# Performance work log

Hardware: AMD Instinct MI355X
Metric: run time of the kernel (lower is better)

The kernel has to match this reference:

```python
import jax, jax.numpy as jnp
import numpy as np

N_NODES = 50000
N_EDGES = 800000
IN_SIZE = 128
HID = 128
OUT_SIZE = 64
N_LAYERS = 2
MAXK = 32


def setup_inputs() -> dict:
    key = jax.random.key(0)
    ks = jax.random.split(key, 8)
    s = 0.05  # small init scale, xavier-like
    return {
        "x": jax.random.normal(ks[0], (N_NODES, IN_SIZE), dtype=jnp.float32),
        "W_in": jax.random.normal(ks[1], (IN_SIZE, HID), dtype=jnp.float32) * s,
        "b_in": jnp.zeros((HID,), dtype=jnp.float32),
        "W_self": jax.random.normal(ks[2], (N_LAYERS, HID, HID), dtype=jnp.float32) * s,
        "W_neigh": jax.random.normal(ks[3], (N_LAYERS, HID, HID), dtype=jnp.float32) * s,
        "W_out": jax.random.normal(ks[4], (HID, OUT_SIZE), dtype=jnp.float32) * s,
        "b_out": jnp.zeros((OUT_SIZE,), dtype=jnp.float32),
        "edge_index": jax.random.randint(ks[5], (2, N_EDGES), 0, N_NODES, dtype=jnp.int32),
        "k": MAXK,
    }


def _maxk(x, k):
    # Keep top-k values per row, zero out the rest (MaxK nonlinearity).
    vals, idx = jax.lax.top_k(x, k)                     # [N, k]
    rows = jnp.arange(x.shape[0])[:, None]
    return jnp.zeros_like(x).at[rows, idx].set(vals)


def reference(x, W_in, b_in, W_self, W_neigh, W_out, b_out, edge_index, k):
    N = x.shape[0]
    src, dst = edge_index[0], edge_index[1]
    # Row sums of the (src->dst) adjacency = out-degree of src, per original code.
    deg = jax.ops.segment_sum(jnp.ones((src.shape[0],), dtype=x.dtype), src,
                              num_segments=N)[:, None]  # [N, 1]
    h = x @ W_in + b_in                                  # lin_in
    for i in range(W_self.shape[0]):
        hs = _maxk(h, k)                                 # MaxK sparsify [N, H]
        # adj @ hs : out[i] = sum over edges (i -> j) of hs[j]; then mean-normalize
        agg = jax.ops.segment_sum(hs[dst], src, num_segments=N) / (deg + 1e-6)
        h = hs @ W_self[i] + agg @ W_neigh[i]            # h_self + h_neigh
        # dropout (eval) and Identity norm are no-ops
    return h @ W_out + b_out                             # lin_out
```

## Files before the change

kernel.cpp:

```cpp
#include <hip/hip_runtime.h>

#define KDIM 128
#define NNODE 50000
#define CHSTRIDE 800000

typedef _Float16 f16x8 __attribute__((ext_vector_type(8)));
typedef _Float16 f16x4 __attribute__((ext_vector_type(4)));
typedef float f32x16 __attribute__((ext_vector_type(16)));

#define NRANGE 6250
#define ECHUNK 3200

__global__ void hist_kernel(const int* __restrict__ src, int* __restrict__ cnt, int E) {
    const int r = blockIdx.x & 7;
    const int chunk = blockIdx.x >> 3;
    const int lo = r * NRANGE, hi = lo + NRANGE;
    const int base = chunk * ECHUNK;
    const int end = min(base + ECHUNK, E);
    for (int i = base + threadIdx.x; i < end; i += 256) {
        int s = src[i];
        if (s >= lo && s < hi) atomicAdd(&cnt[s], 1);
    }
}

__global__ void scatter_kernel(const int* __restrict__ src, const int* __restrict__ dst,
                               int* cursor, int* __restrict__ col, int E) {
    const int r = blockIdx.x & 7;
    const int chunk = blockIdx.x >> 3;
    const int lo = r * NRANGE, hi = lo + NRANGE;
    const int base = chunk * ECHUNK;
    const int end = min(base + ECHUNK, E);
    for (int i = base + threadIdx.x; i < end; i += 256) {
        int s = src[i];
        if (s >= lo && s < hi) {
            int p = atomicAdd(&cursor[s], 1);
            col[p] = dst[i];
        }
    }
}

__global__ void scan1_kernel(const int* __restrict__ cnt, int* __restrict__ row_ptr,
                             int* __restrict__ bsum, int N) {
    __shared__ int ws[4];
    const int t = threadIdx.x;
    const int lane = t & 63, w = t >> 6;
    const int i = blockIdx.x * 256 + t;
    int v = (i < N) ? cnt[i] : 0;
    int x = v;
    #pragma unroll
    for (int off = 1; off < 64; off <<= 1) {
        int u = __shfl_up(x, off);
        if (lane >= off) x += u;
    }
    if (lane == 63) ws[w] = x;
    __syncthreads();
    int wexcl = 0;
    #pragma unroll
    for (int k = 0; k < 4; k++) wexcl += (k < w) ? ws[k] : 0;
    if (i < N) row_ptr[i] = wexcl + x - v;
    if (t == 255) bsum[blockIdx.x] = wexcl + x;
}

__global__ void scan2_kernel(int* __restrict__ bsum, int NB) {
    __shared__ int ws[4];
    const int t = threadIdx.x;
    const int lane = t & 63, w = t >> 6;
    int v = (t < NB) ? bsum[t] : 0;
    int x = v;
    #pragma unroll
    for (int off = 1; off < 64; off <<= 1) {
        int u = __shfl_up(x, off);
        if (lane >= off) x += u;
    }
    if (lane == 63) ws[w] = x;
    __syncthreads();
    int wexcl = 0;
    #pragma unroll
    for (int k = 0; k < 4; k++) wexcl += (k < w) ? ws[k] : 0;
    if (t < NB) bsum[t] = wexcl + x - v;
}

__global__ void scan3_kernel(const int* __restrict__ bsum, int* __restrict__ row_ptr,
                             int* __restrict__ cursor, int N, int E) {
    const int i = blockIdx.x * 256 + threadIdx.x;
    if (i < N) {
        int v = row_ptr[i] + bsum[blockIdx.x];
        row_ptr[i] = v;
        cursor[i] = v;
    }
    if (i == 0) row_ptr[N] = E;
}

__global__ void sortrows_kernel(const int* __restrict__ row_ptr, int* __restrict__ col, int M) {
    int wid = (blockIdx.x * blockDim.x + threadIdx.x) >> 6;
    int lane = threadIdx.x & 63;
    if (wid >= M) return;
    int s = row_ptr[wid], e = row_ptr[wid + 1], len = e - s;
    if (len <= 1) return;
    if (len <= 64) {
        int v = (lane < len) ? col[s + lane] : 0x7fffffff;
        #pragma unroll
        for (int k = 2; k <= 64; k <<= 1) {
            #pragma unroll
            for (int j = k >> 1; j > 0; j >>= 1) {
                int o = __shfl_xor(v, j);
                bool dir = ((lane & k) == 0);
                bool smaller = ((lane & j) == 0);
                int mn = min(v, o), mx = max(v, o);
                v = (dir == smaller) ? mn : mx;
            }
        }
        if (lane < len) col[s + lane] = v;
    } else if (lane == 0) {
        for (int a = s + 1; a < e; a++) {
            int key = col[a];
            int b = a - 1;
            while (b >= s && col[b] > key) { col[b + 1] = col[b]; b--; }
            col[b + 1] = key;
        }
    }
}

__device__ __forceinline__ float2 maxk_row(float2 v, int lane) {
    unsigned int u0 = __float_as_uint(v.x);
    u0 = (u0 & 0x80000000u) ? ~u0 : (u0 | 0x80000000u);
    unsigned int u1 = __float_as_uint(v.y);
    u1 = (u1 & 0x80000000u) ? ~u1 : (u1 | 0x80000000u);

    unsigned int prefix = 0;
    int remaining = 32;
    #pragma unroll
    for (int b = 31; b >= 0; --b) {
        unsigned int candHi = (prefix >> b) | 1u;
        unsigned long long m0 = __ballot((u0 >> b) == candHi);
        unsigned long long m1 = __ballot((u1 >> b) == candHi);
        int cnt = __popcll(m0) + __popcll(m1);
        if (cnt >= remaining) prefix |= (1u << b);
        else remaining -= cnt;
    }

    unsigned long long e0 = __ballot(u0 == prefix);
    unsigned long long e1 = __ballot(u1 == prefix);
    unsigned long long g0 = __ballot(u0 > prefix);
    unsigned long long g1 = __ballot(u1 > prefix);
    int quota = 32 - (__popcll(g0) + __popcll(g1));
    unsigned long long below = (1ULL << lane) - 1ULL;
    int rank0 = __popcll(e0 & below) + __popcll(e1 & below);
    int rank1 = rank0 + (int)((e0 >> lane) & 1ULL);
    bool k0 = (u0 > prefix) || (((e0 >> lane) & 1ULL) && rank0 < quota);
    bool k1 = (u1 > prefix) || (((e1 >> lane) & 1ULL) && rank1 < quota);

    float2 o;
    o.x = k0 ? v.x : 0.0f;
    o.y = k1 ? v.y : 0.0f;
    return o;
}

#define ANPB 16
#define AECAP 1024

__global__ __launch_bounds__(256)
void aggregate_kernel(const float* __restrict__ hsc, const int* __restrict__ row_ptr,
                      const int* __restrict__ col, float* __restrict__ agg, int M) {
    __shared__ int cols[AECAP];
    const int c = blockIdx.x & 7;
    const int g = blockIdx.x >> 3;
    const int n0 = g * ANPB;
    const int tid = threadIdx.x;
    const int w = tid >> 6;
    const int lane = tid & 63;
    const int ng = lane >> 4;
    const int e2 = (lane >> 3) & 1;
    const int f2 = lane & 7;

    const int nend = min(n0 + ANPB, M);
    const int base0 = row_ptr[n0];
    const int ecount = row_ptr[nend] - base0;
    const bool fits = (ecount <= AECAP);
    if (fits) {
        for (int i = tid; i < ecount; i += 256) cols[i] = col[base0 + i];
    }
    __syncthreads();

    const int n = n0 + w * 4 + ng;
    const bool valid = (n < M);
    const int s = valid ? (row_ptr[n] - base0) : 0;
    const int e = valid ? (row_ptr[n + 1] - base0) : 0;
    const char* bp = (const char*)(hsc + (size_t)c * CHSTRIDE) + f2 * 8;

    float ax = 0.f, ay = 0.f, bx = 0.f, by = 0.f;
    int j = s + e2;
    if (fits) {
        for (; j + 2 < e; j += 4) {
            unsigned o0 = (unsigned)cols[j] << 6;
            unsigned o1 = (unsigned)cols[j + 2] << 6;
            float2 v0 = *(const float2*)(bp + o0);
            float2 v1 = *(const float2*)(bp + o1);
            ax += v0.x; ay += v0.y;
            bx += v1.x; by += v1.y;
        }
        if (j < e) {
            float2 v = *(const float2*)(bp + ((unsigned)cols[j] << 6));
            ax += v.x; ay += v.y;
        }
    } else {
        const int* cg = col + base0;
        for (; j + 2 < e; j += 4) {
            unsigned o0 = (unsigned)cg[j] << 6;
            unsigned o1 = (unsigned)cg[j + 2] << 6;
            float2 v0 = *(const float2*)(bp + o0);
            float2 v1 = *(const float2*)(bp + o1);
            ax += v0.x; ay += v0.y;
            bx += v1.x; by += v1.y;
        }
        if (j < e) {
            float2 v = *(const float2*)(bp + ((unsigned)cg[j] << 6));
            ax += v.x; ay += v.y;
        }
    }

    float tx = ax + bx, ty = ay + by;
    tx += __shfl_xor(tx, 8);
    ty += __shfl_xor(ty, 8);
    if (valid && e2 == 0) {
        float inv = 1.0f / ((float)(e - s) + 1e-6f);
        float2 o;
        o.x = tx * inv;
        o.y = ty * inv;
        ((float2*)(agg + (size_t)n * KDIM + c * 16))[f2] = o;
    }
}

__global__ void conv_wt_kernel(const float* __restrict__ W_in,
                               const float* __restrict__ W_self,
                               const float* __restrict__ W_neigh,
                               const float* __restrict__ W_out,
                               _Float16* __restrict__ wb) {
    int t = blockIdx.x * blockDim.x + threadIdx.x;
    if (t < 81920) {
        int m = t >> 14;
        int e = t & 16383;
        int n = e >> 7, k = e & 127;
        const float* S = (m == 0) ? W_in
                       : (m <= 2) ? (W_self + (size_t)(m - 1) * 16384)
                                  : (W_neigh + (size_t)(m - 3) * 16384);
        float v = S[k * 128 + n];
        _Float16 hi = (_Float16)v;
        _Float16 lo = (_Float16)(v - (float)hi);
        int pair = m * 2;
        wb[(size_t)pair * 16384 + n * 128 + k] = hi;
        wb[(size_t)(pair + 1) * 16384 + n * 128 + k] = lo;
    } else if (t < 90112) {
        int e = t - 81920;
        int n = e >> 7, k = e & 127;
        float v = W_out[k * 64 + n];
        _Float16 hi = (_Float16)v;
        _Float16 lo = (_Float16)(v - (float)hi);
        wb[(size_t)10 * 16384 + e] = hi;
        wb[(size_t)11 * 16384 + e] = lo;
    }
}

template <int BN, bool DUAL, bool BIAS, bool A1CHUNK, bool FUSE_MAXK, bool FUSE_OUT>
__global__ __launch_bounds__(256)
void gemm_mfma(const float* __restrict__ A1, const float* __restrict__ A2,
               const _Float16* __restrict__ B1h, const _Float16* __restrict__ B1l,
               const _Float16* __restrict__ B2h, const _Float16* __restrict__ B2l,
               const float* __restrict__ bias, float* __restrict__ C,
               float* __restrict__ hsc_out,
               const _Float16* __restrict__ Oh, const _Float16* __restrict__ Ol,
               const float* __restrict__ obias, float* __restrict__ oout, int M) {
    constexpr int BM = (BN == 128) ? 32 : 64;
    constexpr int NSRC = DUAL ? 2 : 1;
    constexpr int AREG = BM / 8;
    constexpr int LOOFF = BM * 256;

    __shared__ __align__(16) char Alds[2 * BM * 256];

    const int tid = threadIdx.x;
    const int w = tid >> 6;
    const int lane = tid & 63;
    const int l31 = lane & 31;
    const int kslot = lane >> 5;
    const int row0 = blockIdx.x * BM;

    const int n0 = (BN == 128) ? w * 32 : (w & 1) * 32;
    const int mt0 = (BN == 128) ? 0 : (w >> 1);

    const int srow = tid >> 5;
    const int k4 = tid & 31;

    f32x16 acc;
    #pragma unroll
    for (int e = 0; e < 16; e++) acc[e] = 0.0f;

    float4 pa[AREG];
    #pragma unroll
    for (int p = 0; p < AREG; p++) {
        int row = srow + p * 8;
        float4 v = make_float4(0.f, 0.f, 0.f, 0.f);
        if (row0 + row < M) {
            if (A1CHUNK)
                v = *(const float4*)(A1 + (size_t)(k4 >> 2) * CHSTRIDE
                                        + (size_t)(row0 + row) * 16 + (k4 & 3) * 4);
            else
                v = *(const float4*)(A1 + (size_t)(row0 + row) * KDIM + k4 * 4);
        }
        pa[p] = v;
    }

    #pragma unroll
    for (int s = 0; s < NSRC; s++) {
        if (s) __syncthreads();
        const _Float16* Bh = s ? B2h : B1h;
        const _Float16* Bl = s ? B2l : B1l;
        const _Float16* bph = Bh + (size_t)(n0 + l31) * 128 + kslot * 8;
        const _Float16* bpl = Bl + (size_t)(n0 + l31) * 128 + kslot * 8;
        f16x8 bhr[8], blr[8];
        #pragma unroll
        for (int kb = 0; kb < 8; kb++) {
            bhr[kb] = *(const f16x8*)(bph + kb * 16);
            blr[kb] = *(const f16x8*)(bpl + kb * 16);
        }

        #pragma unroll
        for (int p = 0; p < AREG; p++) {
            int row = srow + p * 8;
            float4 v = pa[p];
            _Float16 h0 = (_Float16)v.x, h1 = (_Float16)v.y,
                     h2 = (_Float16)v.z, h3 = (_Float16)v.w;
            f16x4 hv = {h0, h1, h2, h3};
            f16x4 lv = {(_Float16)(v.x - (float)h0), (_Float16)(v.y - (float)h1),
                        (_Float16)(v.z - (float)h2), (_Float16)(v.w - (float)h3)};
            int boff = (k4 * 8) ^ ((row & 7) << 4);
            *(f16x4*)(Alds + row * 256 + boff) = hv;
            *(f16x4*)(Alds + LOOFF + row * 256 + boff) = lv;
        }
        __syncthreads();

        if (s + 1 < NSRC) {
            #pragma unroll
            for (int p = 0; p < AREG; p++) {
                int row = srow + p * 8;
                float4 v = make_float4(0.f, 0.f, 0.f, 0.f);
                if (row0 + row < M)
                    v = *(const float4*)(A2 + (size_t)(row0 + row) * KDIM + k4 * 4);
                pa[p] = v;
            }
        }

        const int arow = mt0 * 32 + l31;
        #pragma unroll
        for (int kb = 0; kb < 8; kb++) {
            int boff = ((kb * 2 + kslot) * 16) ^ ((arow & 7) << 4);
            const char* rp = Alds + arow * 256 + boff;
            f16x8 ah = *(const f16x8*)(rp);
            f16x8 al = *(const f16x8*)(rp + LOOFF);
            acc = __builtin_amdgcn_mfma_f32_32x32x16_f16(al, bhr[kb], acc, 0, 0, 0);
            acc = __builtin_amdgcn_mfma_f32_32x32x16_f16(ah, blr[kb], acc, 0, 0, 0);
            acc = __builtin_amdgcn_mfma_f32_32x32x16_f16(ah, bhr[kb], acc, 0, 0, 0);
        }
    }

    float bv = 0.0f;
    if (BIAS) bv = bias[n0 + l31];

    if constexpr (FUSE_MAXK) {
        __syncthreads();
        float* ht = (float*)Alds;
        #pragma unroll
        for (int r = 0; r < 16; r++) {
            int row = (r & 3) + 8 * (r >> 2) + 4 * kslot;
            ht[row * 128 + n0 + l31] = acc[r] + bv;
        }
        __syncthreads();
        float* slab = hsc_out + (size_t)(lane >> 3) * CHSTRIDE;
        #pragma unroll 1
        for (int rr = 0; rr < BM / 4; rr++) {
            int row = w * (BM / 4) + rr;
            float2 v = *(const float2*)(ht + row * 128 + lane * 2);
            float2 o = maxk_row(v, lane);
            int n = row0 + row;
            if (n < M)
                ((float2*)slab)[(size_t)n * 8 + (lane & 7)] = o;
        }
    } else if constexpr (FUSE_OUT) {
        __syncthreads();
        float* ht = (float*)Alds;
        const int colg = n0 + l31;
        const int c4w = colg >> 2, cw = colg & 3;
        #pragma unroll
        for (int r = 0; r < 16; r++) {
            int row = (r & 3) + 8 * (r >> 2) + 4 * kslot;
            ht[row * 128 + (((c4w ^ (row & 7)) << 2) + cw)] = acc[r];
        }
        __syncthreads();
        if (w < 2) {
            const int ow = w * 32 + l31;
            const _Float16* oph = Oh + (size_t)ow * 128 + kslot * 8;
            const _Float16* opl = Ol + (size_t)ow * 128 + kslot * 8;
            f16x8 obh[8], obl[8];
            #pragma unroll
            for (int kb = 0; kb < 8; kb++) {
                obh[kb] = *(const f16x8*)(oph + kb * 16);
                obl[kb] = *(const f16x8*)(opl + kb * 16);
            }
            f32x16 acc2;
            #pragma unroll
            for (int e = 0; e < 16; e++) acc2[e] = 0.0f;
            const float* hrow = ht + l31 * 128;
            const int hx = l31 & 7;
            #pragma unroll
            for (int kb = 0; kb < 8; kb++) {
                int c4a = kb * 4 + kslot * 2;
                float4 f0 = *(const float4*)(hrow + (((c4a)     ^ hx) << 2));
                float4 f1 = *(const float4*)(hrow + (((c4a + 1) ^ hx) << 2));
                _Float16 h0 = (_Float16)f0.x, h1 = (_Float16)f0.y,
                         h2 = (_Float16)f0.z, h3 = (_Float16)f0.w,
                         h4 = (_Float16)f1.x, h5 = (_Float16)f1.y,
                         h6 = (_Float16)f1.z, h7 = (_Float16)f1.w;
                f16x8 ah = {h0, h1, h2, h3, h4, h5, h6, h7};
                f16x8 al = {(_Float16)(f0.x - (float)h0), (_Float16)(f0.y - (float)h1),
                            (_Float16)(f0.z - (float)h2), (_Float16)(f0.w - (float)h3),
                            (_Float16)(f1.x - (float)h4), (_Float16)(f1.y - (float)h5),
                            (_Float16)(f1.z - (float)h6), (_Float16)(f1.w - (float)h7)};
                acc2 = __builtin_amdgcn_mfma_f32_32x32x16_f16(al, obh[kb], acc2, 0, 0, 0);
                acc2 = __builtin_amdgcn_mfma_f32_32x32x16_f16(ah, obl[kb], acc2, 0, 0, 0);
                acc2 = __builtin_amdgcn_mfma_f32_32x32x16_f16(ah, obh[kb], acc2, 0, 0, 0);
            }
            const float ob = obias[ow];
            #pragma unroll
            for (int r = 0; r < 16; r++) {
                int row = row0 + (r & 3) + 8 * (r >> 2) + 4 * kslot;
                if (row < M) oout[(size_t)row * 64 + ow] = acc2[r] + ob;
            }
        }
    } else {
        #pragma unroll
        for (int r = 0; r < 16; r++) {
            int row = row0 + mt0 * 32 + (r & 3) + 8 * (r >> 2) + 4 * kslot;
            if (row < M) C[(size_t)row * BN + n0 + l31] = acc[r] + bv;
        }
    }
}

extern "C" void kernel_launch(void* const* d_in, const int* in_sizes, int n_in,
                              void* d_out, int out_size, void* d_ws, size_t ws_size,
                              hipStream_t stream) {
    const float* x       = (const float*)d_in[0];
    const float* W_in    = (const float*)d_in[1];
    const float* b_in    = (const float*)d_in[2];
    const float* W_self  = (const float*)d_in[3];
    const float* W_neigh = (const float*)d_in[4];
    const float* W_out   = (const float*)d_in[5];
    const float* b_out   = (const float*)d_in[6];
    const int*   eidx    = (const int*)d_in[7];

    const int N = NNODE, E = 800000;
    const int* src = eidx;
    const int* dst = eidx + E;

    char* ws = (char*)d_ws;
    float* slabA = (float*)(ws);
    float* slabB = (float*)(ws + 25600000);
    float* agg   = (float*)(ws + 51200000);
    int* cnt     = (int*)(ws + 76800000);
    int* row_ptr = (int*)(ws + 77000000);
    int* cursor  = (int*)(ws + 77200016);
    int* col     = (int*)(ws + 77400016);
    _Float16* wb = (_Float16*)(ws + 80600016);
    int* bsum    = (int*)(ws + 81000016);

    const _Float16* WinT_h  = wb + (size_t)0 * 16384;
    const _Float16* WinT_l  = wb + (size_t)1 * 16384;
    const _Float16* WoutT_h = wb + (size_t)10 * 16384;
    const _Float16* WoutT_l = wb + (size_t)11 * 16384;

    const int NB = (N + 255) / 256;
    const int EG = ((E + ECHUNK - 1) / ECHUNK) * 8;
    const int AG = ((N + ANPB - 1) / ANPB) * 8;
    const int G32 = (N + 31) / 32;

    hipMemsetAsync(cnt, 0, N * sizeof(int), stream);
    hist_kernel<<<EG, 256, 0, stream>>>(src, cnt, E);
    scan1_kernel<<<NB, 256, 0, stream>>>(cnt, row_ptr, bsum, N);
    scan2_kernel<<<1, 256, 0, stream>>>(bsum, NB);
    scan3_kernel<<<NB, 256, 0, stream>>>(bsum, row_ptr, cursor, N, E);
    scatter_kernel<<<EG, 256, 0, stream>>>(src, dst, cursor, col, E);
    sortrows_kernel<<<(N + 3) / 4, 256, 0, stream>>>(row_ptr, col, N);
    conv_wt_kernel<<<(90112 + 255) / 256, 256, 0, stream>>>(W_in, W_self, W_neigh, W_out, wb);

    gemm_mfma<128, false, true, false, true, false><<<G32, 256, 0, stream>>>(
        x, nullptr, WinT_h, WinT_l, nullptr, nullptr, b_in, nullptr, slabA,
        nullptr, nullptr, nullptr, nullptr, N);

    aggregate_kernel<<<AG, 256, 0, stream>>>(slabA, row_ptr, col, agg, N);
    gemm_mfma<128, true, false, true, true, false><<<G32, 256, 0, stream>>>(
        slabA, agg, wb + (size_t)2 * 16384, wb + (size_t)3 * 16384,
        wb + (size_t)6 * 16384, wb + (size_t)7 * 16384, nullptr, nullptr, slabB,
        nullptr, nullptr, nullptr, nullptr, N);

    aggregate_kernel<<<AG, 256, 0, stream>>>(slabB, row_ptr, col, agg, N);
    gemm_mfma<128, true, false, true, false, true><<<G32, 256, 0, stream>>>(
        slabB, agg, wb + (size_t)4 * 16384, wb + (size_t)5 * 16384,
        wb + (size_t)8 * 16384, wb + (size_t)9 * 16384, nullptr, nullptr, nullptr,
        WoutT_h, WoutT_l, b_out, (float*)d_out, N);
}
```

Before: 355.3 us.

## Fuse neighbor aggregation into dual GEMM and switch hs to row-major layout

Removes the standalone aggregate kernel and the agg buffer. Each 32-row GEMM block now gathers neighbor rows of hs itself, accumulates the means in registers, and writes them into shared memory as the second MFMA operand. The hs slab changes from a channel-chunked layout to plain row-major, so gathers use float4 reads of whole 512-byte rows. This saves two launches and the agg write/read traffic, but the aggregation parallelism drops from 8 chunk blocks per node group to one block per 32 rows. That can cut memory-level parallelism and occupancy during the gather phase.

```diff
diff --git a/kernel.cpp b/kernel.cpp
--- a/kernel.cpp
+++ b/kernel.cpp
@@ -2,7 +2,6 @@
 
 #define KDIM 128
 #define NNODE 50000
-#define CHSTRIDE 800000
 
 typedef _Float16 f16x8 __attribute__((ext_vector_type(8)));
 typedef _Float16 f16x4 __attribute__((ext_vector_type(4)));
@@ -154,81 +153,6 @@
     o.x = k0 ? v.x : 0.0f;
     o.y = k1 ? v.y : 0.0f;
     return o;
-}
-
-#define ANPB 16
-#define AECAP 1024
-
-__global__ __launch_bounds__(256)
-void aggregate_kernel(const float* __restrict__ hsc, const int* __restrict__ row_ptr,
-                      const int* __restrict__ col, float* __restrict__ agg, int M) {
-    __shared__ int cols[AECAP];
-    const int c = blockIdx.x & 7;
-    const int g = blockIdx.x >> 3;
-    const int n0 = g * ANPB;
-    const int tid = threadIdx.x;
-    const int w = tid >> 6;
-    const int lane = tid & 63;
-    const int ng = lane >> 4;
-    const int e2 = (lane >> 3) & 1;
-    const int f2 = lane & 7;
-
-    const int nend = min(n0 + ANPB, M);
-    const int base0 = row_ptr[n0];
-    const int ecount = row_ptr[nend] - base0;
-    const bool fits = (ecount <= AECAP);
-    if (fits) {
-        for (int i = tid; i < ecount; i += 256) cols[i] = col[base0 + i];
-    }
-    __syncthreads();
-
-    const int n = n0 + w * 4 + ng;
-    const bool valid = (n < M);
-    const int s = valid ? (row_ptr[n] - base0) : 0;
-    const int e = valid ? (row_ptr[n + 1] - base0) : 0;
-    const char* bp = (const char*)(hsc + (size_t)c * CHSTRIDE) + f2 * 8;
-
-    float ax = 0.f, ay = 0.f, bx = 0.f, by = 0.f;
-    int j = s + e2;
-    if (fits) {
-        for (; j + 2 < e; j += 4) {
-            unsigned o0 = (unsigned)cols[j] << 6;
-            unsigned o1 = (unsigned)cols[j + 2] << 6;
-            float2 v0 = *(const float2*)(bp + o0);
-            float2 v1 = *(const float2*)(bp + o1);
-            ax += v0.x; ay += v0.y;
-            bx += v1.x; by += v1.y;
-        }
-        if (j < e) {
-            float2 v = *(const float2*)(bp + ((unsigned)cols[j] << 6));
-            ax += v.x; ay += v.y;
-        }
-    } else {
-        const int* cg = col + base0;
-        for (; j + 2 < e; j += 4) {
-            unsigned o0 = (unsigned)cg[j] << 6;
-            unsigned o1 = (unsigned)cg[j + 2] << 6;
-            float2 v0 = *(const float2*)(bp + o0);
-            float2 v1 = *(const float2*)(bp + o1);
-            ax += v0.x; ay += v0.y;
-            bx += v1.x; by += v1.y;
-        }
-        if (j < e) {
-            float2 v = *(const float2*)(bp + ((unsigned)cg[j] << 6));
-            ax += v.x; ay += v.y;
-        }
-    }
-
-    float tx = ax + bx, ty = ay + by;
-    tx += __shfl_xor(tx, 8);
-    ty += __shfl_xor(ty, 8);
-    if (valid && e2 == 0) {
-        float inv = 1.0f / ((float)(e - s) + 1e-6f);
-        float2 o;
-        o.x = tx * inv;
-        o.y = ty * inv;
-        ((float2*)(agg + (size_t)n * KDIM + c * 16))[f2] = o;
-    }
 }
 
 __global__ void conv_wt_kernel(const float* __restrict__ W_in,
@@ -261,31 +185,29 @@
     }
 }
 
-template <int BN, bool DUAL, bool BIAS, bool A1CHUNK, bool FUSE_MAXK, bool FUSE_OUT>
+template <bool FUSE_AGG, bool BIAS, bool FUSE_MAXK>
 __global__ __launch_bounds__(256)
-void gemm_mfma(const float* __restrict__ A1, const float* __restrict__ A2,
+void gemm_mfma(const float* __restrict__ A1,
                const _Float16* __restrict__ B1h, const _Float16* __restrict__ B1l,
                const _Float16* __restrict__ B2h, const _Float16* __restrict__ B2l,
-               const float* __restrict__ bias, float* __restrict__ C,
-               float* __restrict__ hsc_out,
+               const int* __restrict__ row_ptr, const int* __restrict__ col,
+               const float* __restrict__ bias,
+               float* __restrict__ hs_out,
                const _Float16* __restrict__ Oh, const _Float16* __restrict__ Ol,
                const float* __restrict__ obias, float* __restrict__ oout, int M) {
-    constexpr int BM = (BN == 128) ? 32 : 64;
-    constexpr int NSRC = DUAL ? 2 : 1;
-    constexpr int AREG = BM / 8;
-    constexpr int LOOFF = BM * 256;
-
-    __shared__ __align__(16) char Alds[2 * BM * 256];
+    constexpr int NSRC = FUSE_AGG ? 2 : 1;
+    constexpr int LOOFF = 32 * 256;
+
+    __shared__ __align__(16) char Alds[2 * 32 * 256];
+    __shared__ int cols[FUSE_AGG ? 1024 : 1];
 
     const int tid = threadIdx.x;
     const int w = tid >> 6;
     const int lane = tid & 63;
     const int l31 = lane & 31;
     const int kslot = lane >> 5;
-    const int row0 = blockIdx.x * BM;
-
-    const int n0 = (BN == 128) ? w * 32 : (w & 1) * 32;
-    const int mt0 = (BN == 128) ? 0 : (w >> 1);
+    const int row0 = blockIdx.x * 32;
+    const int n0 = w * 32;
 
     const int srow = tid >> 5;
     const int k4 = tid & 31;
@@ -294,19 +216,89 @@
     #pragma unroll
     for (int e = 0; e < 16; e++) acc[e] = 0.0f;
 
-    float4 pa[AREG];
-    #pragma unroll
-    for (int p = 0; p < AREG; p++) {
+    float4 pa[4];
+    #pragma unroll
+    for (int p = 0; p < 4; p++) {
         int row = srow + p * 8;
         float4 v = make_float4(0.f, 0.f, 0.f, 0.f);
-        if (row0 + row < M) {
-            if (A1CHUNK)
-                v = *(const float4*)(A1 + (size_t)(k4 >> 2) * CHSTRIDE
-                                        + (size_t)(row0 + row) * 16 + (k4 & 3) * 4);
-            else
-                v = *(const float4*)(A1 + (size_t)(row0 + row) * KDIM + k4 * 4);
-        }
+        if (row0 + row < M)
+            v = *(const float4*)(A1 + (size_t)(row0 + row) * KDIM + k4 * 4);
         pa[p] = v;
+    }
+
+    float4 ru[8];
+    if constexpr (FUSE_AGG) {
+        const int nend = min(row0 + 32, M);
+        const int base0 = row_ptr[row0];
+        const int ecount = row_ptr[nend] - base0;
+        const bool fits = (ecount <= 1024);
+        if (fits) {
+            for (int i = tid; i < ecount; i += 256) cols[i] = col[base0 + i];
+        }
+        __syncthreads();
+        const float4* hp = (const float4*)A1;
+        #pragma unroll
+        for (int u = 0; u < 8; u++) {
+            int n = row0 + w * 8 + u;
+            float4 t = make_float4(0.f, 0.f, 0.f, 0.f);
+            float invd = 0.0f;
+            if (n < M) {
+                int s = row_ptr[n] - base0, e = row_ptr[n + 1] - base0;
+                float4 a0 = make_float4(0.f, 0.f, 0.f, 0.f);
+                float4 a1 = a0, a2 = a0, a3 = a0;
+                int j = s + kslot;
+                if (fits) {
+                    for (; j + 6 < e; j += 8) {
+                        int c0 = cols[j];     int c1 = cols[j + 2];
+                        int c2 = cols[j + 4]; int c3 = cols[j + 6];
+                        float4 v0 = hp[(size_t)c0 * 32 + l31];
+                        float4 v1 = hp[(size_t)c1 * 32 + l31];
+                        float4 v2 = hp[(size_t)c2 * 32 + l31];
+                        float4 v3 = hp[(size_t)c3 * 32 + l31];
+                        a0.x += v0.x; a0.y += v0.y; a0.z += v0.z; a0.w += v0.w;
+                        a1.x += v1.x; a1.y += v1.y; a1.z += v1.z; a1.w += v1.w;
+                        a2.x += v2.x; a2.y += v2.y; a2.z += v2.z; a2.w += v2.w;
+                        a3.x += v3.x; a3.y += v3.y; a3.z += v3.z; a3.w += v3.w;
+                    }
+                    for (; j < e; j += 2) {
+                        float4 v = hp[(size_t)cols[j] * 32 + l31];
+                        a0.x += v.x; a0.y += v.y; a0.z += v.z; a0.w += v.w;
+                    }
+                } else {
+                    const int* cg = col + base0;
+                    for (; j + 6 < e; j += 8) {
+                        int c0 = cg[j];     int c1 = cg[j + 2];
+                        int c2 = cg[j + 4]; int c3 = cg[j + 6];
+                        float4 v0 = hp[(size_t)c0 * 32 + l31];
+                        float4 v1 = hp[(size_t)c1 * 32 + l31];
+                        float4 v2 = hp[(size_t)c2 * 32 + l31];
+                        float4 v3 = hp[(size_t)c3 * 32 + l31];
+                        a0.x += v0.x; a0.y += v0.y; a0.z += v0.z; a0.w += v0.w;
+                        a1.x += v1.x; a1.y += v1.y; a1.z += v1.z; a1.w += v1.w;
+                        a2.x += v2.x; a2.y += v2.y; a2.z += v2.z; a2.w += v2.w;
+                        a3.x += v3.x; a3.y += v3.y; a3.z += v3.z; a3.w += v3.w;
+                    }
+                    for (; j < e; j += 2) {
+                        float4 v = hp[(size_t)cg[j] * 32 + l31];
+                        a0.x += v.x; a0.y += v.y; a0.z += v.z; a0.w += v.w;
+                    }
+                }
+                t.x = ((a0.x + a1.x) + a2.x) + a3.x;
+                t.y = ((a0.y + a1.y) + a2.y) + a3.y;
+                t.z = ((a0.z + a1.z) + a2.z) + a3.z;
+                t.w = ((a0.w + a1.w) + a2.w) + a3.w;
+                invd = 1.0f / ((float)(e - s) + 1e-6f);
+            }
+            float4 uo;
+            uo.x = __shfl_xor(t.x, 32);
+            uo.y = __shfl_xor(t.y, 32);
+            uo.z = __shfl_xor(t.z, 32);
+            uo.w = __shfl_xor(t.w, 32);
+            ru[u].x = (t.x + uo.x) * invd;
+            ru[u].y = (t.y + uo.y) * invd;
+            ru[u].z = (t.z + uo.z) * invd;
+            ru[u].w = (t.w + uo.w) * invd;
+        }
     }
 
     #pragma unroll
@@ -323,33 +315,40 @@
             blr[kb] = *(const f16x8*)(bpl + kb * 16);
         }
 
-        #pragma unroll
-        for (int p = 0; p < AREG; p++) {
-            int row = srow + p * 8;
-            float4 v = pa[p];
-            _Float16 h0 = (_Float16)v.x, h1 = (_Float16)v.y,
-                     h2 = (_Float16)v.z, h3 = (_Float16)v.w;
-            f16x4 hv = {h0, h1, h2, h3};
-            f16x4 lv = {(_Float16)(v.x - (float)h0), (_Float16)(v.y - (float)h1),
-                        (_Float16)(v.z - (float)h2), (_Float16)(v.w - (float)h3)};
-            int boff = (k4 * 8) ^ ((row & 7) << 4);
-            *(f16x4*)(Alds + row * 256 + boff) = hv;
-            *(f16x4*)(Alds + LOOFF + row * 256 + boff) = lv;
-        }
-        __syncthreads();
-
-        if (s + 1 < NSRC) {
-            #pragma unroll
-            for (int p = 0; p < AREG; p++) {
+        if (s == 0) {
+            #pragma unroll
+            for (int p = 0; p < 4; p++) {
                 int row = srow + p * 8;
-                float4 v = make_float4(0.f, 0.f, 0.f, 0.f);
-                if (row0 + row < M)
-                    v = *(const float4*)(A2 + (size_t)(row0 + row) * KDIM + k4 * 4);
-                pa[p] = v;
-            }
-        }
-
-        const int arow = mt0 * 32 + l31;
+                float4 v = pa[p];
+                _Float16 h0 = (_Float16)v.x, h1 = (_Float16)v.y,
+                         h2 = (_Float16)v.z, h3 = (_Float16)v.w;
+                f16x4 hv = {h0, h1, h2, h3};
+                f16x4 lv = {(_Float16)(v.x - (float)h0), (_Float16)(v.y - (float)h1),
+                            (_Float16)(v.z - (float)h2), (_Float16)(v.w - (float)h3)};
+                int boff = (k4 * 8) ^ ((row & 7) << 4);
+                *(f16x4*)(Alds + row * 256 + boff) = hv;
+                *(f16x4*)(Alds + LOOFF + row * 256 + boff) = lv;
+            }
+        } else {
+            #pragma unroll
+            for (int u = 0; u < 8; u++) {
+                if (kslot == 0) {
+                    int row = w * 8 + u;
+                    float4 v = ru[u];
+                    _Float16 h0 = (_Float16)v.x, h1 = (_Float16)v.y,
+                             h2 = (_Float16)v.z, h3 = (_Float16)v.w;
+                    f16x4 hv = {h0, h1, h2, h3};
+                    f16x4 lv = {(_Float16)(v.x - (float)h0), (_Float16)(v.y - (float)h1),
+                                (_Float16)(v.z - (float)h2), (_Float16)(v.w - (float)h3)};
+                    int boff = (l31 * 8) ^ ((row & 7) << 4);
+                    *(f16x4*)(Alds + row * 256 + boff) = hv;
+                    *(f16x4*)(Alds + LOOFF + row * 256 + boff) = lv;
+                }
+            }
+        }
+        __syncthreads();
+
+        const int arow = l31;
         #pragma unroll
         for (int kb = 0; kb < 8; kb++) {
             int boff = ((kb * 2 + kslot) * 16) ^ ((arow & 7) << 4);
@@ -374,17 +373,16 @@
             ht[row * 128 + n0 + l31] = acc[r] + bv;
         }
         __syncthreads();
-        float* slab = hsc_out + (size_t)(lane >> 3) * CHSTRIDE;
         #pragma unroll 1
-        for (int rr = 0; rr < BM / 4; rr++) {
-            int row = w * (BM / 4) + rr;
+        for (int rr = 0; rr < 8; rr++) {
+            int row = w * 8 + rr;
             float2 v = *(const float2*)(ht + row * 128 + lane * 2);
             float2 o = maxk_row(v, lane);
             int n = row0 + row;
             if (n < M)
-                ((float2*)slab)[(size_t)n * 8 + (lane & 7)] = o;
-        }
-    } else if constexpr (FUSE_OUT) {
+                ((float2*)hs_out)[(size_t)n * 64 + lane] = o;
+        }
+    } else {
         __syncthreads();
         float* ht = (float*)Alds;
         const int colg = n0 + l31;
@@ -435,12 +433,6 @@
                 if (row < M) oout[(size_t)row * 64 + ow] = acc2[r] + ob;
             }
         }
-    } else {
-        #pragma unroll
-        for (int r = 0; r < 16; r++) {
-            int row = row0 + mt0 * 32 + (r & 3) + 8 * (r >> 2) + 4 * kslot;
-            if (row < M) C[(size_t)row * BN + n0 + l31] = acc[r] + bv;
-        }
     }
 }
 
@@ -463,7 +455,6 @@
     char* ws = (char*)d_ws;
     float* slabA = (float*)(ws);
     float* slabB = (float*)(ws + 25600000);
-    float* agg   = (float*)(ws + 51200000);
     int* cnt     = (int*)(ws + 76800000);
     int* row_ptr = (int*)(ws + 77000000);
     int* cursor  = (int*)(ws + 77200016);
@@ -478,7 +469,6 @@
 
     const int NB = (N + 255) / 256;
     const int EG = ((E + ECHUNK - 1) / ECHUNK) * 8;
-    const int AG = ((N + ANPB - 1) / ANPB) * 8;
     const int G32 = (N + 31) / 32;
 
     hipMemsetAsync(cnt, 0, N * sizeof(int), stream);
@@ -490,19 +480,17 @@
     sortrows_kernel<<<(N + 3) / 4, 256, 0, stream>>>(row_ptr, col, N);
     conv_wt_kernel<<<(90112 + 255) / 256, 256, 0, stream>>>(W_in, W_self, W_neigh, W_out, wb);
 
-    gemm_mfma<128, false, true, false, true, false><<<G32, 256, 0, stream>>>(
-        x, nullptr, WinT_h, WinT_l, nullptr, nullptr, b_in, nullptr, slabA,
-        nullptr, nullptr, nullptr, nullptr, N);
-
-    aggregate_kernel<<<AG, 256, 0, stream>>>(slabA, row_ptr, col, agg, N);
-    gemm_mfma<128, true, false, true, true, false><<<G32, 256, 0, stream>>>(
-        slabA, agg, wb + (size_t)2 * 16384, wb + (size_t)3 * 16384,
-        wb + (size_t)6 * 16384, wb + (size_t)7 * 16384, nullptr, nullptr, slabB,
-        nullptr, nullptr, nullptr, nullptr, N);
-
-    aggregate_kernel<<<AG, 256, 0, stream>>>(slabB, row_ptr, col, agg, N);
-    gemm_mfma<128, true, false, true, false, true><<<G32, 256, 0, stream>>>(
-        slabB, agg, wb + (size_t)4 * 16384, wb + (size_t)5 * 16384,
-        wb + (size_t)8 * 16384, wb + (size_t)9 * 16384, nullptr, nullptr, nullptr,
-        WoutT_h, WoutT_l, b_out, (float*)d_out, N);
-}
+    gemm_mfma<false, true, true><<<G32, 256, 0, stream>>>(
+        x, WinT_h, WinT_l, nullptr, nullptr, nullptr, nullptr, b_in,
+        slabA, nullptr, nullptr, nullptr, nullptr, N);
+
+    gemm_mfma<true, false, true><<<G32, 256, 0, stream>>>(
+        slabA, wb + (size_t)2 * 16384, wb + (size_t)3 * 16384,
+        wb + (size_t)6 * 16384, wb + (size_t)7 * 16384, row_ptr, col, nullptr,
+        slabB, nullptr, nullptr, nullptr, nullptr, N);
+
+    gemm_mfma<true, false, false><<<G32, 256, 0, stream>>>(
+        slabB, wb + (size_t)4 * 16384, wb + (size_t)5 * 16384,
+        wb + (size_t)8 * 16384, wb + (size_t)9 * 16384, row_ptr, col, nullptr,
+        nullptr, WoutT_h, WoutT_l, b_out, (float*)d_out, N);
+}
```

After: 387.2 us. 1.09x slower.
